# Optimization experiments

Hardware: AMD Instinct MI355X
Metric: run time of the kernel (lower is better)

## Reference

```python
import jax, jax.numpy as jnp
import numpy as np

EMB = 64
HID = 128
N_NODES = 50000
N_EDGES = 800000
N_Q = 64

def setup_inputs() -> dict:
    key = jax.random.key(0)
    ks = jax.random.split(key, 20)
    d = {}
    d['question_emb'] = jax.random.normal(ks[0], (N_Q, EMB), dtype=jnp.float32)
    d['node_embeddings'] = jax.random.normal(ks[1], (N_NODES, EMB), dtype=jnp.float32)
    d['edge_embeddings'] = jax.random.normal(ks[2], (N_EDGES, EMB), dtype=jnp.float32)
    d['edge_index'] = jax.random.randint(ks[3], (2, N_EDGES), 0, N_NODES, dtype=jnp.int32)
    d['node_batch'] = jnp.sort(jax.random.randint(ks[4], (N_NODES,), 0, N_Q, dtype=jnp.int32))
    s = 1.0 / np.sqrt(EMB)
    # projector weights (Linear emb->emb), stored as (in, out)
    d['Wq'] = jax.random.normal(ks[5], (EMB, EMB), dtype=jnp.float32) * s
    d['bq'] = jnp.zeros((EMB,), dtype=jnp.float32)
    d['We'] = jax.random.normal(ks[6], (EMB, EMB), dtype=jnp.float32) * s
    d['be'] = jnp.zeros((EMB,), dtype=jnp.float32)
    d['Wr'] = jax.random.normal(ks[7], (EMB, EMB), dtype=jnp.float32) * s
    d['br'] = jnp.zeros((EMB,), dtype=jnp.float32)
    # DenseFeatureExtractor: concat(4*EMB) -> EMB -> HID, ReLU after each
    d['W1'] = jax.random.normal(ks[8], (4 * EMB, EMB), dtype=jnp.float32) / np.sqrt(4 * EMB)
    d['b1'] = jnp.zeros((EMB,), dtype=jnp.float32)
    d['W2'] = jax.random.normal(ks[9], (EMB, HID), dtype=jnp.float32) * s
    d['b2'] = jnp.zeros((HID,), dtype=jnp.float32)
    # DeterministicHead: HID -> 1
    d['Wh'] = jax.random.normal(ks[10], (HID, 1), dtype=jnp.float32) / np.sqrt(HID)
    d['bh'] = jnp.zeros((1,), dtype=jnp.float32)
    return d


def reference(question_emb, node_embeddings, edge_embeddings, edge_index, node_batch,
              Wq, bq, We, be, Wr, br, W1, b1, W2, b2, Wh, bh):
    head_idx, tail_idx = edge_index[0], edge_index[1]
    query_ids = node_batch[head_idx]                       # [E]
    # projections (applied to the small tables, then gathered per edge)
    q_repr = question_emb @ Wq + bq                        # [Q, D]
    node_repr = node_embeddings @ We + be                  # [N, D]
    rel_repr = edge_embeddings @ Wr + br                   # [E, D]
    semantic = jnp.concatenate([
        q_repr[query_ids], node_repr[head_idx], rel_repr, node_repr[tail_idx]
    ], axis=-1)                                            # [E, 4D]
    h = jax.nn.relu(semantic @ W1 + b1)                    # [E, D]
    h = jax.nn.relu(h @ W2 + b2)                           # [E, H]
    logits = (h @ Wh + bh)[:, 0]                           # [E]
    scores = jax.nn.sigmoid(logits)
    return scores
```

## Files before the change

### kernel.cpp

```cpp
#include <hip/hip_runtime.h>

#define NNODE 50000
#define NEDGE 800000

typedef __attribute__((ext_vector_type(8))) short bf16x8;
typedef __attribute__((ext_vector_type(4))) float f32x4;

#define WB_QCB   0
#define WB_WRTB  8192
#define WB_W2SB  16384
#define WB_WEH   32768
#define WB_WET   49152
#define WB_NHB   65536
#define WB_NTB   6465536
#define WB_EIDX  12865536

__device__ inline ushort f2b(float x) {
    uint u = __float_as_uint(x);
    return (ushort)((u + 0x7fffu + ((u >> 16) & 1u)) >> 16);
}
__device__ inline uint pack2(float lo, float hi) {
    uint a = __float_as_uint(lo);
    uint b = __float_as_uint(hi);
    a += 0x7fffu + ((a >> 16) & 1u);
    b += 0x7fffu + ((b >> 16) & 1u);
    return __builtin_amdgcn_perm(b, a, 0x07060302);
}
__device__ inline float bLo(uint u) { return __uint_as_float(u << 16); }
__device__ inline float bHi(uint u) { return __uint_as_float(u & 0xffff0000u); }

__device__ inline float row16_reduce(float v) {
    int x;
    x = __builtin_amdgcn_mov_dpp(__float_as_int(v), 0x121, 0xf, 0xf, false); v += __int_as_float(x);
    x = __builtin_amdgcn_mov_dpp(__float_as_int(v), 0x122, 0xf, 0xf, false); v += __int_as_float(x);
    x = __builtin_amdgcn_mov_dpp(__float_as_int(v), 0x124, 0xf, 0xf, false); v += __int_as_float(x);
    x = __builtin_amdgcn_mov_dpp(__float_as_int(v), 0x128, 0xf, 0xf, false); v += __int_as_float(x);
    return v;
}

union B8U { uint4 u; bf16x8 b; };

__device__ inline void stage64(float* dst, const float* __restrict__ src, int t) {
    #pragma unroll
    for (int i = 0; i < 4; ++i) {
        int f = t + i * 256;
        *(float4*)&dst[f * 4] = *(const float4*)&src[f * 4];
    }
}

__device__ inline void gemm64(const float* sA, const float* sB, int t, float acc[4][4]) {
    const int r0 = (t >> 4) * 4, c0 = (t & 15) * 4;
    #pragma unroll
    for (int j = 0; j < 4; ++j)
        #pragma unroll
        for (int i = 0; i < 4; ++i) acc[j][i] = 0.f;
    #pragma unroll 4
    for (int k = 0; k < 64; ++k) {
        float4 b = *(const float4*)&sB[k * 64 + c0];
        float bv[4] = {b.x, b.y, b.z, b.w};
        #pragma unroll
        for (int j = 0; j < 4; ++j) {
            float a = sA[(r0 + j) * 64 + k];
            #pragma unroll
            for (int i = 0; i < 4; ++i) acc[j][i] = fmaf(a, bv[i], acc[j][i]);
        }
    }
}

__global__ __launch_bounds__(256)
void prep_a(const float* __restrict__ Q,
            const float* __restrict__ Wq, const float* __restrict__ bq,
            const float* __restrict__ We, const float* __restrict__ be,
            const float* __restrict__ Wr, const float* __restrict__ br,
            const float* __restrict__ W1, const float* __restrict__ b1,
            const float* __restrict__ W2,
            const int* __restrict__ EI, const int* __restrict__ NB,
            char* __restrict__ wsb)
{
    __shared__ float sA[4096], sB[4096], sC[4096], sBias[64];
    const int t = threadIdx.x;
    const int bid = blockIdx.x;
    const int r0 = (t >> 4) * 4, c0 = (t & 15) * 4;

    if (bid >= 5) {
        int e0 = (bid - 5) * 1024 + t * 4;
        if (e0 < NEDGE) {
            int4 hds = *(const int4*)&EI[e0];
            int4 tls = *(const int4*)&EI[NEDGE + e0];
            int4* eidx = (int4*)(wsb + WB_EIDX);
            eidx[e0 + 0] = make_int4(hds.x, tls.x, NB[hds.x], 0);
            eidx[e0 + 1] = make_int4(hds.y, tls.y, NB[hds.y], 0);
            eidx[e0 + 2] = make_int4(hds.z, tls.z, NB[hds.z], 0);
            eidx[e0 + 3] = make_int4(hds.w, tls.w, NB[hds.w], 0);
        }
        return;
    }

    if (bid == 0) {
        stage64(sA, Wq, t); stage64(sB, W1, t);
        __syncthreads();
        float acc[4][4];
        gemm64(sA, sB, t, acc);
        #pragma unroll
        for (int j = 0; j < 4; ++j)
            *(float4*)&sC[(r0 + j) * 64 + c0] = make_float4(acc[j][0], acc[j][1], acc[j][2], acc[j][3]);
        if (t < 64) {
            float s = b1[t];
            for (int k = 0; k < 64; ++k) {
                s = fmaf(bq[k], W1[k * 64 + t], s);
                s = fmaf(be[k], W1[(64 + k) * 64 + t] + W1[(192 + k) * 64 + t], s);
                s = fmaf(br[k], W1[(128 + k) * 64 + t], s);
            }
            sBias[t] = s;
        }
        __syncthreads();
        stage64(sA, Q, t);
        __syncthreads();
        gemm64(sA, sC, t, acc);
        ushort* qcb = (ushort*)(wsb + WB_QCB);
        #pragma unroll
        for (int j = 0; j < 4; ++j) {
            ushort4 p;
            p.x = f2b(acc[j][0] + sBias[c0 + 0]);
            p.y = f2b(acc[j][1] + sBias[c0 + 1]);
            p.z = f2b(acc[j][2] + sBias[c0 + 2]);
            p.w = f2b(acc[j][3] + sBias[c0 + 3]);
            *(ushort4*)&qcb[(r0 + j) * 64 + c0] = p;
        }
    } else if (bid == 1 || bid == 2) {
        const float* w1seg = W1 + (bid == 1 ? 64 * 64 : 192 * 64);
        float* dst = (float*)(wsb + (bid == 1 ? WB_WEH : WB_WET));
        stage64(sA, We, t); stage64(sB, w1seg, t);
        __syncthreads();
        float acc[4][4];
        gemm64(sA, sB, t, acc);
        #pragma unroll
        for (int j = 0; j < 4; ++j)
            *(float4*)&dst[(r0 + j) * 64 + c0] = make_float4(acc[j][0], acc[j][1], acc[j][2], acc[j][3]);
    } else if (bid == 3) {
        stage64(sA, Wr, t); stage64(sB, W1 + 128 * 64, t);
        __syncthreads();
        float acc[4][4];
        gemm64(sA, sB, t, acc);
        ushort* wrtb = (ushort*)(wsb + WB_WRTB);
        #pragma unroll
        for (int j = 0; j < 4; ++j)
            #pragma unroll
            for (int i = 0; i < 4; ++i)
                wrtb[(c0 + i) * 64 + (r0 + j)] = f2b(acc[j][i]);
    } else {
        ushort* w2s = (ushort*)(wsb + WB_W2SB);
        #pragma unroll
        for (int i = 0; i < 32; ++i) {
            int f = t + i * 256;
            int k = f >> 7, n = f & 127;
            int p = (k & 15) * 4 + (k >> 4);
            w2s[n * 64 + (((p >> 3) ^ (n & 7)) * 8) + (p & 7)] = f2b(W2[f]);
        }
    }
}

__global__ __launch_bounds__(256)
void prep_nodes(const float* __restrict__ Xn, const char* __restrict__ wsb_c,
                char* __restrict__ wsb)
{
    __shared__ float sXT[64 * 68];
    __shared__ float sWeh[4096], sWet[4096];
    const int t = threadIdx.x;
    const int nbase = blockIdx.x * 64;
    const float* Weh = (const float*)(wsb_c + WB_WEH);
    const float* Wet = (const float*)(wsb_c + WB_WET);
    ushort* nhb = (ushort*)(wsb + WB_NHB);
    ushort* ntb = (ushort*)(wsb + WB_NTB);

    #pragma unroll
    for (int i = 0; i < 4; ++i) {
        int f = t + i * 256;
        int n = f >> 4, s4 = (f & 15) * 4;
        int gn = nbase + n;
        float4 v = make_float4(0.f, 0.f, 0.f, 0.f);
        if (gn < NNODE) v = *(const float4*)&Xn[gn * 64 + s4];
        sXT[(s4 + 0) * 68 + n] = v.x;
        sXT[(s4 + 1) * 68 + n] = v.y;
        sXT[(s4 + 2) * 68 + n] = v.z;
        sXT[(s4 + 3) * 68 + n] = v.w;
    }
    #pragma unroll
    for (int i = 0; i < 4; ++i) {
        int f = t + i * 256;
        *(float4*)&sWeh[f * 4] = *(const float4*)&Weh[f * 4];
        *(float4*)&sWet[f * 4] = *(const float4*)&Wet[f * 4];
    }
    __syncthreads();

    const int er = (t >> 4) * 4, cc = (t & 15) * 4;
    float ah[4][4], at[4][4];
    #pragma unroll
    for (int j = 0; j < 4; ++j)
        #pragma unroll
        for (int i = 0; i < 4; ++i) { ah[j][i] = 0.f; at[j][i] = 0.f; }
    #pragma unroll 4
    for (int k = 0; k < 64; ++k) {
        float4 a  = *(const float4*)&sXT[k * 68 + er];
        float4 bh = *(const float4*)&sWeh[k * 64 + cc];
        float4 bt = *(const float4*)&sWet[k * 64 + cc];
        float av[4] = {a.x, a.y, a.z, a.w};
        #pragma unroll
        for (int j = 0; j < 4; ++j) {
            ah[j][0] = fmaf(av[j], bh.x, ah[j][0]); ah[j][1] = fmaf(av[j], bh.y, ah[j][1]);
            ah[j][2] = fmaf(av[j], bh.z, ah[j][2]); ah[j][3] = fmaf(av[j], bh.w, ah[j][3]);
            at[j][0] = fmaf(av[j], bt.x, at[j][0]); at[j][1] = fmaf(av[j], bt.y, at[j][1]);
            at[j][2] = fmaf(av[j], bt.z, at[j][2]); at[j][3] = fmaf(av[j], bt.w, at[j][3]);
        }
    }
    #pragma unroll
    for (int j = 0; j < 4; ++j) {
        int n = nbase + er + j;
        if (n < NNODE) {
            ushort4 ph, pt;
            ph.x = f2b(ah[j][0]); ph.y = f2b(ah[j][1]); ph.z = f2b(ah[j][2]); ph.w = f2b(ah[j][3]);
            pt.x = f2b(at[j][0]); pt.y = f2b(at[j][1]); pt.z = f2b(at[j][2]); pt.w = f2b(at[j][3]);
            *(ushort4*)&nhb[n * 64 + cc] = ph;
            *(ushort4*)&ntb[n * 64 + cc] = pt;
        }
    }
}

__global__ __launch_bounds__(256, 6)
void edge_kernel(const float* __restrict__ Xe,
                 const float* __restrict__ b2,
                 const float* __restrict__ Wh,
                 const float* __restrict__ bh,
                 const char* __restrict__ wsb,
                 float* __restrict__ out)
{
    __shared__ ushort sW2[128 * 64];
    __shared__ ushort sG[64 * 72];
    __shared__ float  sB2s[128], sWhs[128];

    const int t = threadIdx.x;
    const int ebase = blockIdx.x * 64;
    const int l = t & 63, w = t >> 6;
    const int m = l & 15, qq = l >> 4, q8 = qq * 8;

    const ushort* qcb  = (const ushort*)(wsb + WB_QCB);
    const ushort* wrtb = (const ushort*)(wsb + WB_WRTB);
    const ushort* w2s  = (const ushort*)(wsb + WB_W2SB);
    const ushort* nhb  = (const ushort*)(wsb + WB_NHB);
    const ushort* ntb  = (const ushort*)(wsb + WB_NTB);
    const int4*   eidx = (const int4*)(wsb + WB_EIDX);

    const int eg = w * 16 + (l >> 2);
    const int qg = l & 3;
    int4 idx = eidx[ebase + eg];

    const float* xrow = &Xe[(size_t)(ebase + w * 16 + m) * 64];
    float4 x0 = *(const float4*)&xrow[q8];
    float4 x1 = *(const float4*)&xrow[q8 + 4];
    float4 x2 = *(const float4*)&xrow[32 + q8];
    float4 x3 = *(const float4*)&xrow[32 + q8 + 4];

    #pragma unroll
    for (int i = 0; i < 4; ++i) {
        int f = t + i * 256;
        *(uint4*)&sW2[f * 8] = *(const uint4*)&w2s[f * 8];
    }
    if (t < 128) { sB2s[t] = b2[t]; sWhs[t] = Wh[t]; }
    float bh0 = bh[0];

    {
        const int hd = idx.x, tl = idx.y, qi = idx.z;
        float s[16];
        #pragma unroll
        for (int a = 0; a < 4; ++a) {
            int coff = a * 16 + qg * 4;
            uint2 gq = *(const uint2*)&qcb[qi * 64 + coff];
            uint2 gh = *(const uint2*)&nhb[(size_t)hd * 64 + coff];
            uint2 gt = *(const uint2*)&ntb[(size_t)tl * 64 + coff];
            s[a]      = bLo(gq.x) + bLo(gh.x) + bLo(gt.x);
            s[4 + a]  = bHi(gq.x) + bHi(gh.x) + bHi(gt.x);
            s[8 + a]  = bLo(gq.y) + bLo(gh.y) + bLo(gt.y);
            s[12 + a] = bHi(gq.y) + bHi(gh.y) + bHi(gt.y);
        }
        uint pk[8];
        #pragma unroll
        for (int wd = 0; wd < 8; ++wd) pk[wd] = pack2(s[2 * wd], s[2 * wd + 1]);
        *(uint4*)&sG[eg * 72 + qg * 16]     = make_uint4(pk[0], pk[1], pk[2], pk[3]);
        *(uint4*)&sG[eg * 72 + qg * 16 + 8] = make_uint4(pk[4], pk[5], pk[6], pk[7]);
    }

    B8U a0, a1;
    a0.u = make_uint4(pack2(x0.x, x0.y), pack2(x0.z, x0.w),
                      pack2(x1.x, x1.y), pack2(x1.z, x1.w));
    a1.u = make_uint4(pack2(x2.x, x2.y), pack2(x2.z, x2.w),
                      pack2(x3.x, x3.y), pack2(x3.z, x3.w));

    __syncthreads();

    f32x4 acc1[4];
    #pragma unroll
    for (int nt = 0; nt < 4; ++nt) {
        const ushort* row = &wrtb[(nt * 16 + m) * 64];
        B8U b0, b1v;
        b0.u  = *(const uint4*)&row[q8];
        b1v.u = *(const uint4*)&row[32 + q8];
        f32x4 c = {0.f, 0.f, 0.f, 0.f};
        c = __builtin_amdgcn_mfma_f32_16x16x32_bf16(a0.b, b0.b, c, 0, 0, 0);
        c = __builtin_amdgcn_mfma_f32_16x16x32_bf16(a1.b, b1v.b, c, 0, 0, 0);
        acc1[nt] = c;
    }

    #pragma unroll
    for (int r = 0; r < 4; ++r) {
        int e = w * 16 + qq * 4 + r;
        uint2 gg = *(const uint2*)&sG[e * 72 + m * 4];
        uint lo = pack2(fmaxf(acc1[0][r] + bLo(gg.x), 0.f),
                        fmaxf(acc1[1][r] + bHi(gg.x), 0.f));
        uint hi = pack2(fmaxf(acc1[2][r] + bLo(gg.y), 0.f),
                        fmaxf(acc1[3][r] + bHi(gg.y), 0.f));
        *(uint2*)&sG[e * 72 + m * 4] = make_uint2(lo, hi);
    }

    bf16x8 A0 = *(const bf16x8*)&sG[(w * 16 + m) * 72 + q8];
    bf16x8 A1 = *(const bf16x8*)&sG[(w * 16 + m) * 72 + 32 + q8];
    const int o1 = (qq ^ (m & 7)) * 8;
    const int o2 = o1 ^ 32;
    float part[4] = {0.f, 0.f, 0.f, 0.f};
    #pragma unroll
    for (int nt = 0; nt < 8; ++nt) {
        B8U B0, B1;
        B0.u = *(const uint4*)&sW2[nt * 1024 + m * 64 + o1];
        B1.u = *(const uint4*)&sW2[nt * 1024 + m * 64 + o2];
        f32x4 c = {0.f, 0.f, 0.f, 0.f};
        c = __builtin_amdgcn_mfma_f32_16x16x32_bf16(A0, B0.b, c, 0, 0, 0);
        c = __builtin_amdgcn_mfma_f32_16x16x32_bf16(A1, B1.b, c, 0, 0, 0);
        int col = nt * 16 + m;
        float b2v = sB2s[col], whv = sWhs[col];
        #pragma unroll
        for (int r = 0; r < 4; ++r)
            part[r] = fmaf(fmaxf(c[r] + b2v, 0.f), whv, part[r]);
    }

    part[0] = row16_reduce(part[0]);
    part[1] = row16_reduce(part[1]);
    part[2] = row16_reduce(part[2]);
    part[3] = row16_reduce(part[3]);

    if (m == 0) {
        float4 o;
        o.x = 1.f / (1.f + __expf(-(part[0] + bh0)));
        o.y = 1.f / (1.f + __expf(-(part[1] + bh0)));
        o.z = 1.f / (1.f + __expf(-(part[2] + bh0)));
        o.w = 1.f / (1.f + __expf(-(part[3] + bh0)));
        *(float4*)&out[ebase + w * 16 + qq * 4] = o;
    }
}

extern "C" void kernel_launch(void* const* d_in, const int* in_sizes, int n_in,
                              void* d_out, int out_size, void* d_ws, size_t ws_size,
                              hipStream_t stream)
{
    const float* Q   = (const float*)d_in[0];
    const float* Xn  = (const float*)d_in[1];
    const float* Xe  = (const float*)d_in[2];
    const int*   EI  = (const int*)d_in[3];
    const int*   NB  = (const int*)d_in[4];
    const float* Wq  = (const float*)d_in[5];
    const float* bq  = (const float*)d_in[6];
    const float* We  = (const float*)d_in[7];
    const float* be  = (const float*)d_in[8];
    const float* Wr  = (const float*)d_in[9];
    const float* br  = (const float*)d_in[10];
    const float* W1  = (const float*)d_in[11];
    const float* b1  = (const float*)d_in[12];
    const float* W2  = (const float*)d_in[13];
    const float* b2  = (const float*)d_in[14];
    const float* Wh  = (const float*)d_in[15];
    const float* bh  = (const float*)d_in[16];
    float* out = (float*)d_out;
    char*  wsb = (char*)d_ws;

    prep_a<<<5 + (NEDGE + 1023) / 1024, 256, 0, stream>>>(
        Q, Wq, bq, We, be, Wr, br, W1, b1, W2, EI, NB, wsb);
    prep_nodes<<<(NNODE + 63) / 64, 256, 0, stream>>>(Xn, wsb, wsb);
    edge_kernel<<<NEDGE / 64, 256, 0, stream>>>(Xe, b2, Wh, bh, wsb, out);
}
```

Before: 408.0 us.

## Fold gathered node/query contributions into layer-1 accumulators via identity MFMAs

Each lane now gathers full bf16 rows for the query, head and tail precomputed contributions in MFMA A-operand layout. Those rows are added into the layer-1 accumulators by multiplying with identity-pattern B fragments, so the VALU sums, bf16 packing and shared-memory staging of the summed gather are no longer needed. This adds twelve extra MFMAs per wave and moves the gathers to a row-per-lane pattern. Launch bounds also drop from 6 to 4 blocks per CU, which lets each thread hold more registers at the cost of occupancy.

```diff
diff --git a/kernel.cpp b/kernel.cpp
--- a/kernel.cpp
+++ b/kernel.cpp
@@ -26,8 +26,6 @@
     b += 0x7fffu + ((b >> 16) & 1u);
     return __builtin_amdgcn_perm(b, a, 0x07060302);
 }
-__device__ inline float bLo(uint u) { return __uint_as_float(u << 16); }
-__device__ inline float bHi(uint u) { return __uint_as_float(u & 0xffff0000u); }
 
 __device__ inline float row16_reduce(float v) {
     int x;
@@ -226,7 +224,7 @@
     }
 }
 
-__global__ __launch_bounds__(256, 6)
+__global__ __launch_bounds__(256, 4)
 void edge_kernel(const float* __restrict__ Xe,
                  const float* __restrict__ b2,
                  const float* __restrict__ Wh,
@@ -235,7 +233,7 @@
                  float* __restrict__ out)
 {
     __shared__ ushort sW2[128 * 64];
-    __shared__ ushort sG[64 * 72];
+    __shared__ ushort sH[64 * 72];
     __shared__ float  sB2s[128], sWhs[128];
 
     const int t = threadIdx.x;
@@ -250,16 +248,23 @@
     const ushort* ntb  = (const ushort*)(wsb + WB_NTB);
     const int4*   eidx = (const int4*)(wsb + WB_EIDX);
 
-    const int eg = w * 16 + (l >> 2);
-    const int qg = l & 3;
-    int4 idx = eidx[ebase + eg];
-
-    const float* xrow = &Xe[(size_t)(ebase + w * 16 + m) * 64];
+    const int erow = w * 16 + m;
+    int4 idx = eidx[ebase + erow];
+
+    const float* xrow = &Xe[(size_t)(ebase + erow) * 64];
     float4 x0 = *(const float4*)&xrow[q8];
     float4 x1 = *(const float4*)&xrow[q8 + 4];
     float4 x2 = *(const float4*)&xrow[32 + q8];
     float4 x3 = *(const float4*)&xrow[32 + q8 + 4];
 
+    const ushort* qrow = &qcb[(size_t)idx.z * 64];
+    const ushort* hrow = &nhb[(size_t)idx.x * 64];
+    const ushort* trow = &ntb[(size_t)idx.y * 64];
+    B8U gq0, gq1, gh0, gh1, gt0, gt1;
+    gq0.u = *(const uint4*)&qrow[q8];      gq1.u = *(const uint4*)&qrow[32 + q8];
+    gh0.u = *(const uint4*)&hrow[q8];      gh1.u = *(const uint4*)&hrow[32 + q8];
+    gt0.u = *(const uint4*)&trow[q8];      gt1.u = *(const uint4*)&trow[32 + q8];
+
     #pragma unroll
     for (int i = 0; i < 4; ++i) {
         int f = t + i * 256;
@@ -268,25 +273,17 @@
     if (t < 128) { sB2s[t] = b2[t]; sWhs[t] = Wh[t]; }
     float bh0 = bh[0];
 
+    B8U Ilo, Ihi;
     {
-        const int hd = idx.x, tl = idx.y, qi = idx.z;
-        float s[16];
-        #pragma unroll
-        for (int a = 0; a < 4; ++a) {
-            int coff = a * 16 + qg * 4;
-            uint2 gq = *(const uint2*)&qcb[qi * 64 + coff];
-            uint2 gh = *(const uint2*)&nhb[(size_t)hd * 64 + coff];
-            uint2 gt = *(const uint2*)&ntb[(size_t)tl * 64 + coff];
-            s[a]      = bLo(gq.x) + bLo(gh.x) + bLo(gt.x);
-            s[4 + a]  = bHi(gq.x) + bHi(gh.x) + bHi(gt.x);
-            s[8 + a]  = bLo(gq.y) + bLo(gh.y) + bLo(gt.y);
-            s[12 + a] = bHi(gq.y) + bHi(gh.y) + bHi(gt.y);
-        }
-        uint pk[8];
-        #pragma unroll
-        for (int wd = 0; wd < 8; ++wd) pk[wd] = pack2(s[2 * wd], s[2 * wd + 1]);
-        *(uint4*)&sG[eg * 72 + qg * 16]     = make_uint4(pk[0], pk[1], pk[2], pk[3]);
-        *(uint4*)&sG[eg * 72 + qg * 16 + 8] = make_uint4(pk[4], pk[5], pk[6], pk[7]);
+        uint lo[4], hi[4];
+        #pragma unroll
+        for (int p = 0; p < 4; ++p) {
+            int k0 = q8 + 2 * p;
+            lo[p] = ((k0 == m) ? 0x3f80u : 0u) | ((k0 + 1 == m) ? 0x3f800000u : 0u);
+            hi[p] = ((k0 == 16 + m) ? 0x3f80u : 0u) | ((k0 + 1 == 16 + m) ? 0x3f800000u : 0u);
+        }
+        Ilo.u = make_uint4(lo[0], lo[1], lo[2], lo[3]);
+        Ihi.u = make_uint4(hi[0], hi[1], hi[2], hi[3]);
     }
 
     B8U a0, a1;
@@ -309,20 +306,29 @@
         c = __builtin_amdgcn_mfma_f32_16x16x32_bf16(a1.b, b1v.b, c, 0, 0, 0);
         acc1[nt] = c;
     }
+    acc1[0] = __builtin_amdgcn_mfma_f32_16x16x32_bf16(gq0.b, Ilo.b, acc1[0], 0, 0, 0);
+    acc1[0] = __builtin_amdgcn_mfma_f32_16x16x32_bf16(gh0.b, Ilo.b, acc1[0], 0, 0, 0);
+    acc1[0] = __builtin_amdgcn_mfma_f32_16x16x32_bf16(gt0.b, Ilo.b, acc1[0], 0, 0, 0);
+    acc1[1] = __builtin_amdgcn_mfma_f32_16x16x32_bf16(gq0.b, Ihi.b, acc1[1], 0, 0, 0);
+    acc1[1] = __builtin_amdgcn_mfma_f32_16x16x32_bf16(gh0.b, Ihi.b, acc1[1], 0, 0, 0);
+    acc1[1] = __builtin_amdgcn_mfma_f32_16x16x32_bf16(gt0.b, Ihi.b, acc1[1], 0, 0, 0);
+    acc1[2] = __builtin_amdgcn_mfma_f32_16x16x32_bf16(gq1.b, Ilo.b, acc1[2], 0, 0, 0);
+    acc1[2] = __builtin_amdgcn_mfma_f32_16x16x32_bf16(gh1.b, Ilo.b, acc1[2], 0, 0, 0);
+    acc1[2] = __builtin_amdgcn_mfma_f32_16x16x32_bf16(gt1.b, Ilo.b, acc1[2], 0, 0, 0);
+    acc1[3] = __builtin_amdgcn_mfma_f32_16x16x32_bf16(gq1.b, Ihi.b, acc1[3], 0, 0, 0);
+    acc1[3] = __builtin_amdgcn_mfma_f32_16x16x32_bf16(gh1.b, Ihi.b, acc1[3], 0, 0, 0);
+    acc1[3] = __builtin_amdgcn_mfma_f32_16x16x32_bf16(gt1.b, Ihi.b, acc1[3], 0, 0, 0);
 
     #pragma unroll
     for (int r = 0; r < 4; ++r) {
         int e = w * 16 + qq * 4 + r;
-        uint2 gg = *(const uint2*)&sG[e * 72 + m * 4];
-        uint lo = pack2(fmaxf(acc1[0][r] + bLo(gg.x), 0.f),
-                        fmaxf(acc1[1][r] + bHi(gg.x), 0.f));
-        uint hi = pack2(fmaxf(acc1[2][r] + bLo(gg.y), 0.f),
-                        fmaxf(acc1[3][r] + bHi(gg.y), 0.f));
-        *(uint2*)&sG[e * 72 + m * 4] = make_uint2(lo, hi);
-    }
-
-    bf16x8 A0 = *(const bf16x8*)&sG[(w * 16 + m) * 72 + q8];
-    bf16x8 A1 = *(const bf16x8*)&sG[(w * 16 + m) * 72 + 32 + q8];
+        uint lo = pack2(fmaxf(acc1[0][r], 0.f), fmaxf(acc1[1][r], 0.f));
+        uint hi = pack2(fmaxf(acc1[2][r], 0.f), fmaxf(acc1[3][r], 0.f));
+        *(uint2*)&sH[e * 72 + m * 4] = make_uint2(lo, hi);
+    }
+
+    bf16x8 A0 = *(const bf16x8*)&sH[(w * 16 + m) * 72 + q8];
+    bf16x8 A1 = *(const bf16x8*)&sH[(w * 16 + m) * 72 + 32 + q8];
     const int o1 = (qq ^ (m & 7)) * 8;
     const int o2 = o1 ^ 32;
     float part[4] = {0.f, 0.f, 0.f, 0.f};
```

Result: faster. 394.5 us (-3.3%).
